# Kernel optimization log

Measured on AMD Instinct MI355X. Metric: run time of the kernel, lower is better.

The kernel has to match this reference:

```python
import jax, jax.numpy as jnp
import numpy as np

N_STEPS = 5


def setup_inputs() -> dict:
    key = jax.random.key(0)
    ks = jax.random.split(key, 12)
    B, N, E, D = 4, 2048, 2, 128
    prop_state = jax.random.normal(ks[0], (B, N, D), dtype=jnp.float32)
    A = (jax.random.uniform(ks[1], (B, N, 2 * N * E)) < 0.01).astype(jnp.float32)
    s = 0.02  # init scale from _initialization
    W_in = jax.random.normal(ks[2], (E, D, D), dtype=jnp.float32) * s
    b_in = jax.random.normal(ks[3], (E, D), dtype=jnp.float32) * s
    W_out = jax.random.normal(ks[4], (E, D, D), dtype=jnp.float32) * s
    b_out = jax.random.normal(ks[5], (E, D), dtype=jnp.float32) * s
    W_r = jax.random.normal(ks[6], (3 * D, D), dtype=jnp.float32) * s
    b_r = jax.random.normal(ks[7], (D,), dtype=jnp.float32) * s
    W_z = jax.random.normal(ks[8], (3 * D, D), dtype=jnp.float32) * s
    b_z = jax.random.normal(ks[9], (D,), dtype=jnp.float32) * s
    W_h = jax.random.normal(ks[10], (3 * D, D), dtype=jnp.float32) * s
    b_h = jax.random.normal(ks[11], (D,), dtype=jnp.float32) * s
    return {"prop_state": prop_state, "A": A, "W_in": W_in, "b_in": b_in,
            "W_out": W_out, "b_out": b_out, "W_r": W_r, "b_r": b_r,
            "W_z": W_z, "b_z": b_z, "W_h": W_h, "b_h": b_h}


def _ggnn_forward(prop_state, A, W_in, b_in, W_out, b_out,
                  W_r, b_r, W_z, b_z, W_h, b_h):
    B, N, D = prop_state.shape
    E = W_in.shape[0]
    A_in = A[:, :, : N * E]    # [B, N, N*E]
    A_out = A[:, :, N * E:]    # [B, N, N*E]
    h = prop_state
    for _ in range(N_STEPS):
        # per-edge-type projections, node-major / edge-type-minor ordering
        ins = (jnp.einsum('bnd,edf->bnef', h, W_in) + b_in).reshape(B, N * E, D)
        outs = (jnp.einsum('bnd,edf->bnef', h, W_out) + b_out).reshape(B, N * E, D)
        a_in = jnp.einsum('bnm,bmd->bnd', A_in, ins)    # [B, N, D]
        a_out = jnp.einsum('bnm,bmd->bnd', A_out, outs)  # [B, N, D]
        a = jnp.concatenate([a_in, a_out, h], axis=-1)   # [B, N, 3D]
        r = jax.nn.sigmoid(a @ W_r + b_r)
        z = jax.nn.sigmoid(a @ W_z + b_z)
        joined = jnp.concatenate([a_in, a_out, r * h], axis=-1)
        h_hat = jnp.tanh(joined @ W_h + b_h)
        h = (1.0 - z) * h + z * h_hat
    return h


def reference(prop_state, A, W_in, b_in, W_out, b_out,
              W_r, b_r, W_z, b_z, W_h, b_h):
    return _ggnn_forward(prop_state, A, W_in, b_in, W_out, b_out,
                         W_r, b_r, W_z, b_z, W_h, b_h)
```

## Files before the change

kernel.cpp:

```cpp
#include <hip/hip_runtime.h>
#include <stdint.h>

#define ROWS 8192
#define CAP 64
#define NSTEPS 5
#define ZROW 8192

typedef short bf16x8 __attribute__((ext_vector_type(8)));
typedef float f32x4 __attribute__((ext_vector_type(4)));
typedef unsigned short u16;
typedef unsigned int u32;

__device__ __forceinline__ float bf2f(u16 u){ union{u32 i; float f;} x; x.i=(u32)u<<16; return x.f; }
__device__ __forceinline__ u16 f2bf(float f){ union{float f; u32 i;} x; x.f=f; u32 r = x.i + 0x7fffu + ((x.i>>16)&1u); return (u16)(r>>16); }

#define MFMA __builtin_amdgcn_mfma_f32_16x16x32_bf16
#define SWZ(r, byte) ((byte) ^ (((r)&7)<<4))


__device__ __forceinline__ float wsel(const float* __restrict__ Wr, const float* __restrict__ Wz,
                                      const float* __restrict__ Wh, int f, int o){
  if (o < 128) return Wr[(size_t)f*128 + o];
  if (o < 256) return Wz[(size_t)f*128 + (o-128)];
  return (f < 256) ? Wh[(size_t)f*128 + (o-256)] : 0.f;
}

__global__ void k_prep(const float* __restrict__ prop, float* __restrict__ hf, u16* __restrict__ hbf,
                       const float* __restrict__ W_in, const float* __restrict__ b_in,
                       const float* __restrict__ W_out, const float* __restrict__ b_out,
                       const float* __restrict__ W_r, const float* __restrict__ W_z,
                       const float* __restrict__ W_h,
                       u16* __restrict__ WfT, float* __restrict__ bv, u16* __restrict__ WhbT)
{
  int bid = blockIdx.x;
  if (bid < 4096){
    int i = bid*256 + threadIdx.x;
    float v = prop[i]; hf[i] = v; hbf[i] = f2bf(v);
    return;
  }
  if (bid == 4096 && threadIdx.x < 128) hbf[(size_t)ZROW*128 + threadIdx.x] = 0;
  int i = (bid-4096)*256 + threadIdx.x;
  if (i < 640*384){
    int k = i/384, o = i - k*384;
    float s;
    if (k >= 512){
      s = wsel(W_r, W_z, W_h, 256 + (k-512), o);
    } else {
      const float* Wrow; int fb;
      if (k < 256){ Wrow = W_in  + (size_t)((k>>7)&1)*16384 + (size_t)(k&127)*128; fb = 0; }
      else { int kk = k-256; Wrow = W_out + (size_t)(kk>>7)*16384 + (size_t)(kk&127)*128; fb = 128; }
      s = 0.f;
#pragma unroll 8
      for (int f=0; f<128; f++) s += Wrow[f] * wsel(W_r, W_z, W_h, fb+f, o);
    }
    WfT[(size_t)o*640 + k] = f2bf(s);
  } else if (i < 640*384 + 4*384){
    int j = i - 640*384; int q = j / 384, o = j - q*384;
    const float* bp = (q < 2) ? (b_in + q*128) : (b_out + (q-2)*128);
    int fb = (q < 2) ? 0 : 128;
    float s = 0.f;
#pragma unroll 8
    for (int f=0; f<128; f++) s += bp[f] * wsel(W_r, W_z, W_h, fb+f, o);
    bv[j] = s;
  } else if (i < 640*384 + 4*384 + 128*128){
    int j = i - (640*384 + 4*384); int kk = j>>7, o = j&127;
    WhbT[(size_t)o*128 + kk] = f2bf(W_h[(size_t)(256+kk)*128 + o]);
  }
}

__global__ void k_csr(const float* __restrict__ A,
                      int* __restrict__ idx4, int* __restrict__ cnt4)
{
  __shared__ int scnt[4];
  __shared__ int slist[4][CAP];
  int row = blockIdx.x, tid = threadIdx.x;
  if (tid < 4) scnt[tid] = 0;
  __syncthreads();
  const float* ar = A + (size_t)row * 8192;
  int babs = (row>>11)<<11;
  for (int c = tid*4; c < 8192; c += 1024){
    float4 v = *reinterpret_cast<const float4*>(ar + c);
    float vv[4] = {v.x, v.y, v.z, v.w};
#pragma unroll
    for (int j=0;j<4;j++){
      if (vv[j] != 0.f){
        int m = c + j;
        int lst = ((m>>12)<<1) | (m&1);
        int n = (m & 4095) >> 1;
        int p = atomicAdd(&scnt[lst], 1);
        if (p < CAP) slist[lst][p] = babs | n;
      }
    }
  }
  __syncthreads();
  if (tid < 4) cnt4[(row<<2) + tid] = scnt[tid];
  for (int j = tid; j < 4*CAP; j += 256){
    int l = j>>6, p = j&63;
    int c = scnt[l]; if (c > CAP) c = CAP;
    if (p < c) idx4[(((size_t)(row<<2) + l)<<6) + p] = slist[l][p];
  }
}

__global__ __launch_bounds__(512) void k_fused(
    const int* __restrict__ cnt4, const int* __restrict__ idx4,
    const u16* __restrict__ WfT, const float* __restrict__ bv,
    const float* __restrict__ b_r, const float* __restrict__ b_z, const float* __restrict__ b_h,
    const u16* __restrict__ WhbT, float* __restrict__ hf, u16* __restrict__ hbf)
{
  __shared__ u16  X_s[32*512];
  __shared__ u16  rh_s[32*128];
  __shared__ u16  z_s[32*128];
  __shared__ u16  hh_s[32*128];
  __shared__ int  cnts[32][4];

  int tid  = threadIdx.x;
  int wave = tid>>6, lane = tid&63, lr = lane&15, lk = lane>>4;
  int m0 = blockIdx.x*32;

  if (tid < 128) cnts[tid>>2][tid&3] = cnt4[((m0 + (tid>>2))<<2) + (tid&3)];

  const u16* hb = hbf + (lane<<1);
#pragma unroll
  for (int p=0; p<2; p++){
    int base_l = p*64 + wave*8;
    int cc[8], my[8];
#pragma unroll
    for (int j=0;j<8;j++){
      int l = base_l + j;
      int lid = ((m0 + (l>>2))<<2) | (l&3);
      int c = cnt4[lid]; if (c > CAP) c = CAP;
      cc[j] = c;
      my[j] = (lane < c) ? idx4[((size_t)lid<<6) + lane] : ZROW;
    }
    int cmax = 0;
#pragma unroll
    for (int j=0;j<8;j++) cmax = max(cmax, cc[j]);

    float a0[8] = {0,0,0,0,0,0,0,0}, a1[8] = {0,0,0,0,0,0,0,0};
    u32 v[8];
#pragma unroll
    for (int j=0;j<8;j++){
      int n = __shfl(my[j], 0);
      v[j] = *reinterpret_cast<const u32*>(hb + ((size_t)n<<7));
    }
    for (int i=1; i<cmax; i++){
      u32 vn[8];
#pragma unroll
      for (int j=0;j<8;j++){
        int n = __shfl(my[j], i);
        vn[j] = *reinterpret_cast<const u32*>(hb + ((size_t)n<<7));
      }
#pragma unroll
      for (int j=0;j<8;j++){
        union{u32 u; float f;} lo, hi;
        lo.u = v[j]<<16; hi.u = v[j] & 0xffff0000u;
        a0[j] += lo.f; a1[j] += hi.f;
        v[j] = vn[j];
      }
    }
    if (cmax > 0){
#pragma unroll
      for (int j=0;j<8;j++){
        union{u32 u; float f;} lo, hi;
        lo.u = v[j]<<16; hi.u = v[j] & 0xffff0000u;
        a0[j] += lo.f; a1[j] += hi.f;
      }
    }
#pragma unroll
    for (int j=0;j<8;j++){
      int l = base_l + j, rl = l>>2, q = l&3;
      u32 pk = ((u32)f2bf(a1[j])<<16) | (u32)f2bf(a0[j]);
      *reinterpret_cast<u32*>((char*)X_s + SWZ(rl, rl*1024 + q*256 + lane*4)) = pk;
    }
  }
  __syncthreads();

  int n0 = wave*48;
  f32x4 acc[2][3] = {};
  const u16* Ah = hbf + (size_t)(m0+lr)*128 + lk*8;
  const u16* Bw = WfT + (size_t)(n0+lr)*640 + lk*8;
#pragma unroll
  for (int k=0;k<512;k+=32){
    bf16x8 b0 = *reinterpret_cast<const bf16x8*>(Bw + k);
    bf16x8 b1 = *reinterpret_cast<const bf16x8*>(Bw + 16*640 + k);
    bf16x8 b2 = *reinterpret_cast<const bf16x8*>(Bw + 32*640 + k);
#pragma unroll
    for (int mt=0;mt<2;mt++){
      int row = mt*16 + lr;
      bf16x8 a = *reinterpret_cast<const bf16x8*>((const char*)X_s + SWZ(row, row*1024 + (k + lk*8)*2));
      acc[mt][0] = MFMA(a, b0, acc[mt][0], 0,0,0);
      acc[mt][1] = MFMA(a, b1, acc[mt][1], 0,0,0);
      acc[mt][2] = MFMA(a, b2, acc[mt][2], 0,0,0);
    }
  }
#pragma unroll
  for (int k=0;k<128;k+=32){
    bf16x8 b0 = *reinterpret_cast<const bf16x8*>(Bw + 512 + k);
    bf16x8 b1 = *reinterpret_cast<const bf16x8*>(Bw + 16*640 + 512 + k);
    bf16x8 b2 = *reinterpret_cast<const bf16x8*>(Bw + 32*640 + 512 + k);
#pragma unroll
    for (int mt=0;mt<2;mt++){
      bf16x8 a = *reinterpret_cast<const bf16x8*>(Ah + (size_t)mt*16*128 + k);
      acc[mt][0] = MFMA(a, b0, acc[mt][0], 0,0,0);
      acc[mt][1] = MFMA(a, b1, acc[mt][1], 0,0,0);
      acc[mt][2] = MFMA(a, b2, acc[mt][2], 0,0,0);
    }
  }

#pragma unroll
  for (int nt=0;nt<3;nt++){
    int oo = n0 + nt*16 + lr;
    float base = (oo<128) ? b_r[oo] : (oo<256) ? b_z[oo-128] : b_h[oo-256];
    float q0 = bv[oo], q1 = bv[384+oo], q2 = bv[768+oo], q3 = bv[1152+oo];
#pragma unroll
    for (int mt=0;mt<2;mt++){
#pragma unroll
      for (int i2=0;i2<4;i2++){
        int rl = mt*16 + lk*4 + i2;
        float v = acc[mt][nt][i2] + base
                + cnts[rl][0]*q0 + cnts[rl][1]*q1 + cnts[rl][2]*q2 + cnts[rl][3]*q3;
        if (oo < 128){
          float s = 1.f/(1.f + expf(-v));
          float hv = hf[(size_t)(m0+rl)*128 + oo];
          *reinterpret_cast<u16*>((char*)rh_s + SWZ(rl, rl*256 + oo*2)) = f2bf(s*hv);
        } else if (oo < 256){
          float s = 1.f/(1.f + expf(-v));
          z_s[rl*128 + (oo-128)] = (u16)(s*65535.f + 0.5f);
        } else {
          hh_s[rl*128 + (oo-256)] = f2bf(v);
        }
      }
    }
  }
  __syncthreads();

  int c0 = wave*16;
  f32x4 acc2[2] = {};
  const u16* Bh = WhbT + (size_t)(c0+lr)*128 + lk*8;
#pragma unroll
  for (int k=0;k<128;k+=32){
    bf16x8 b = *reinterpret_cast<const bf16x8*>(Bh + k);
#pragma unroll
    for (int mt=0;mt<2;mt++){
      int rr = mt*16 + lr;
      bf16x8 a = *reinterpret_cast<const bf16x8*>((char*)rh_s + SWZ(rr, rr*256 + (k + lk*8)*2));
      acc2[mt] = MFMA(a, b, acc2[mt], 0,0,0);
    }
  }

#pragma unroll
  for (int mt=0;mt<2;mt++){
#pragma unroll
    for (int i2=0;i2<4;i2++){
      int rl = mt*16 + lk*4 + i2, col = c0 + lr;
      size_t ix = (size_t)(m0+rl)*128 + col;
      float hhat = tanhf(acc2[mt][i2] + bf2f(hh_s[rl*128 + col]));
      float zz = (float)z_s[rl*128 + col] * (1.f/65535.f);
      float ho = hf[ix];
      float hn = ho + zz*(hhat - ho);
      hf[ix] = hn;
      hbf[ix] = f2bf(hn);
    }
  }
}


extern "C" void kernel_launch(void* const* d_in, const int* in_sizes, int n_in,
                              void* d_out, int out_size, void* d_ws, size_t ws_size,
                              hipStream_t stream)
{
  const float* prop  = (const float*)d_in[0];
  const float* A     = (const float*)d_in[1];
  const float* W_in  = (const float*)d_in[2];
  const float* b_in  = (const float*)d_in[3];
  const float* W_out = (const float*)d_in[4];
  const float* b_out = (const float*)d_in[5];
  const float* W_r   = (const float*)d_in[6];
  const float* b_r   = (const float*)d_in[7];
  const float* W_z   = (const float*)d_in[8];
  const float* b_z   = (const float*)d_in[9];
  const float* W_h   = (const float*)d_in[10];
  const float* b_h   = (const float*)d_in[11];

  char* ws = (char*)d_ws;
  size_t off = 0;
  auto nxt = [&](size_t bytes)->char*{ char* p = ws + off; off += (bytes + 255) & ~(size_t)255; return p; };
  int*   cnt4  = (int*)  nxt((size_t)ROWS*4*4);
  int*   idx4  = (int*)  nxt((size_t)ROWS*4*CAP*4);
  u16*   hbf   = (u16*)  nxt((size_t)(ROWS+1)*128*2);
  float* hf    = (float*)nxt((size_t)ROWS*128*4);
  u16*   WfT   = (u16*)  nxt((size_t)384*640*2);
  float* bv    = (float*)nxt((size_t)4*384*4);
  u16*   WhbT  = (u16*)  nxt((size_t)128*128*2);

  int fold_blocks = (640*384 + 4*384 + 128*128 + 255)/256;
  k_prep<<<4096 + fold_blocks, 256, 0, stream>>>(prop, hf, hbf,
      W_in, b_in, W_out, b_out, W_r, W_z, W_h, WfT, bv, WhbT);
  k_csr<<<ROWS, 256, 0, stream>>>(A, idx4, cnt4);

  for (int t=0; t<NSTEPS; t++){
    k_fused<<<ROWS/32, 512, 0, stream>>>(cnt4, idx4, WfT, bv, b_r, b_z, b_h, WhbT, hf, hbf);
  }

  hipMemcpyAsync(d_out, hf, (size_t)ROWS*128*4, hipMemcpyDeviceToDevice, stream);
}
```

Measured before the change: 334.2 us.

## Fuse all GGNN steps into one persistent kernel with a grid barrier

Replaces the five per-step kernel launches with a single persistent kernel of 256 blocks that loops over the steps and uses an atomic-counter grid barrier between them. The hidden state is double-buffered so no block reads rows another block is overwriting, and per-row edge counts are read from shared memory instead of global. This removes launch overhead and the gaps between launches, but the spin barrier depends on all 256 blocks being resident at once and adds serialization at each step.

```diff
diff --git a/kernel.cpp b/kernel.cpp
--- a/kernel.cpp
+++ b/kernel.cpp
@@ -5,6 +5,7 @@
 #define CAP 64
 #define NSTEPS 5
 #define ZROW 8192
+#define NBLK 256
 
 typedef short bf16x8 __attribute__((ext_vector_type(8)));
 typedef float f32x4 __attribute__((ext_vector_type(4)));
@@ -25,20 +26,28 @@
   return (f < 256) ? Wh[(size_t)f*128 + (o-256)] : 0.f;
 }
 
-__global__ void k_prep(const float* __restrict__ prop, float* __restrict__ hf, u16* __restrict__ hbf,
+__global__ void k_prep(const float* __restrict__ prop, float* __restrict__ hf0, u16* __restrict__ hbf0,
+                       u16* __restrict__ hbf1,
                        const float* __restrict__ W_in, const float* __restrict__ b_in,
                        const float* __restrict__ W_out, const float* __restrict__ b_out,
                        const float* __restrict__ W_r, const float* __restrict__ W_z,
                        const float* __restrict__ W_h,
-                       u16* __restrict__ WfT, float* __restrict__ bv, u16* __restrict__ WhbT)
+                       u16* __restrict__ WfT, float* __restrict__ bv, u16* __restrict__ WhbT,
+                       int* __restrict__ bar)
 {
   int bid = blockIdx.x;
   if (bid < 4096){
     int i = bid*256 + threadIdx.x;
-    float v = prop[i]; hf[i] = v; hbf[i] = f2bf(v);
+    float v = prop[i]; hf0[i] = v; hbf0[i] = f2bf(v);
     return;
   }
-  if (bid == 4096 && threadIdx.x < 128) hbf[(size_t)ZROW*128 + threadIdx.x] = 0;
+  if (bid == 4096){
+    if (threadIdx.x < 128){
+      hbf0[(size_t)ZROW*128 + threadIdx.x] = 0;
+      hbf1[(size_t)ZROW*128 + threadIdx.x] = 0;
+    }
+    if (threadIdx.x == 255) bar[0] = 0;
+  }
   int i = (bid-4096)*256 + threadIdx.x;
   if (i < 640*384){
     int k = i/384, o = i - k*384;
@@ -101,11 +110,26 @@
   }
 }
 
-__global__ __launch_bounds__(512) void k_fused(
+__device__ __forceinline__ void grid_sync(int* bar, int target){
+  __syncthreads();
+  if (threadIdx.x == 0){
+    __threadfence();
+    __hip_atomic_fetch_add(bar, 1, __ATOMIC_RELEASE, __HIP_MEMORY_SCOPE_AGENT);
+    while (__hip_atomic_fetch_add(bar, 0, __ATOMIC_RELAXED, __HIP_MEMORY_SCOPE_AGENT) < target)
+      __builtin_amdgcn_s_sleep(4);
+    __threadfence();
+  }
+  __syncthreads();
+}
+
+__global__ __launch_bounds__(512) void k_steps(
     const int* __restrict__ cnt4, const int* __restrict__ idx4,
     const u16* __restrict__ WfT, const float* __restrict__ bv,
     const float* __restrict__ b_r, const float* __restrict__ b_z, const float* __restrict__ b_h,
-    const u16* __restrict__ WhbT, float* __restrict__ hf, u16* __restrict__ hbf)
+    const u16* __restrict__ WhbT,
+    float* __restrict__ hf0, float* __restrict__ hf1,
+    u16* __restrict__ hbf0, u16* __restrict__ hbf1,
+    int* __restrict__ bar)
 {
   __shared__ u16  X_s[32*512];
   __shared__ u16  rh_s[32*128];
@@ -118,149 +142,159 @@
   int m0 = blockIdx.x*32;
 
   if (tid < 128) cnts[tid>>2][tid&3] = cnt4[((m0 + (tid>>2))<<2) + (tid&3)];
-
-  const u16* hb = hbf + (lane<<1);
-#pragma unroll
-  for (int p=0; p<2; p++){
-    int base_l = p*64 + wave*8;
-    int cc[8], my[8];
-#pragma unroll
-    for (int j=0;j<8;j++){
-      int l = base_l + j;
-      int lid = ((m0 + (l>>2))<<2) | (l&3);
-      int c = cnt4[lid]; if (c > CAP) c = CAP;
-      cc[j] = c;
-      my[j] = (lane < c) ? idx4[((size_t)lid<<6) + lane] : ZROW;
-    }
-    int cmax = 0;
-#pragma unroll
-    for (int j=0;j<8;j++) cmax = max(cmax, cc[j]);
-
-    float a0[8] = {0,0,0,0,0,0,0,0}, a1[8] = {0,0,0,0,0,0,0,0};
-    u32 v[8];
-#pragma unroll
-    for (int j=0;j<8;j++){
-      int n = __shfl(my[j], 0);
-      v[j] = *reinterpret_cast<const u32*>(hb + ((size_t)n<<7));
-    }
-    for (int i=1; i<cmax; i++){
-      u32 vn[8];
+  __syncthreads();
+
+  for (int step=0; step<NSTEPS; step++){
+    const u16*  hbf_r = (step&1) ? hbf1 : hbf0;
+    u16*        hbf_w = (step&1) ? hbf0 : hbf1;
+    const float* hf_r = (step&1) ? hf1 : hf0;
+    float*       hf_w = (step&1) ? hf0 : hf1;
+
+    const u16* hb = hbf_r + (lane<<1);
+#pragma unroll
+    for (int p=0; p<2; p++){
+      int base_l = p*64 + wave*8;
+      int cc[8], my[8];
 #pragma unroll
       for (int j=0;j<8;j++){
-        int n = __shfl(my[j], i);
-        vn[j] = *reinterpret_cast<const u32*>(hb + ((size_t)n<<7));
-      }
+        int l = base_l + j;
+        int c = cnts[l>>2][l&3]; if (c > CAP) c = CAP;
+        cc[j] = c;
+        int lid = ((m0 + (l>>2))<<2) | (l&3);
+        my[j] = (lane < c) ? idx4[((size_t)lid<<6) + lane] : ZROW;
+      }
+      int cmax = 0;
+#pragma unroll
+      for (int j=0;j<8;j++) cmax = max(cmax, cc[j]);
+
+      float a0[8] = {0,0,0,0,0,0,0,0}, a1[8] = {0,0,0,0,0,0,0,0};
+      u32 v[8];
 #pragma unroll
       for (int j=0;j<8;j++){
-        union{u32 u; float f;} lo, hi;
-        lo.u = v[j]<<16; hi.u = v[j] & 0xffff0000u;
-        a0[j] += lo.f; a1[j] += hi.f;
-        v[j] = vn[j];
-      }
-    }
-    if (cmax > 0){
+        int n = __shfl(my[j], 0);
+        v[j] = *reinterpret_cast<const u32*>(hb + ((size_t)n<<7));
+      }
+      for (int i=1; i<cmax; i++){
+        u32 vn[8];
+#pragma unroll
+        for (int j=0;j<8;j++){
+          int n = __shfl(my[j], i);
+          vn[j] = *reinterpret_cast<const u32*>(hb + ((size_t)n<<7));
+        }
+#pragma unroll
+        for (int j=0;j<8;j++){
+          union{u32 u; float f;} lo, hi;
+          lo.u = v[j]<<16; hi.u = v[j] & 0xffff0000u;
+          a0[j] += lo.f; a1[j] += hi.f;
+          v[j] = vn[j];
+        }
+      }
+      if (cmax > 0){
+#pragma unroll
+        for (int j=0;j<8;j++){
+          union{u32 u; float f;} lo, hi;
+          lo.u = v[j]<<16; hi.u = v[j] & 0xffff0000u;
+          a0[j] += lo.f; a1[j] += hi.f;
+        }
+      }
 #pragma unroll
       for (int j=0;j<8;j++){
-        union{u32 u; float f;} lo, hi;
-        lo.u = v[j]<<16; hi.u = v[j] & 0xffff0000u;
-        a0[j] += lo.f; a1[j] += hi.f;
-      }
-    }
-#pragma unroll
-    for (int j=0;j<8;j++){
-      int l = base_l + j, rl = l>>2, q = l&3;
-      u32 pk = ((u32)f2bf(a1[j])<<16) | (u32)f2bf(a0[j]);
-      *reinterpret_cast<u32*>((char*)X_s + SWZ(rl, rl*1024 + q*256 + lane*4)) = pk;
-    }
-  }
-  __syncthreads();
-
-  int n0 = wave*48;
-  f32x4 acc[2][3] = {};
-  const u16* Ah = hbf + (size_t)(m0+lr)*128 + lk*8;
-  const u16* Bw = WfT + (size_t)(n0+lr)*640 + lk*8;
-#pragma unroll
-  for (int k=0;k<512;k+=32){
-    bf16x8 b0 = *reinterpret_cast<const bf16x8*>(Bw + k);
-    bf16x8 b1 = *reinterpret_cast<const bf16x8*>(Bw + 16*640 + k);
-    bf16x8 b2 = *reinterpret_cast<const bf16x8*>(Bw + 32*640 + k);
+        int l = base_l + j, rl = l>>2, q = l&3;
+        u32 pk = ((u32)f2bf(a1[j])<<16) | (u32)f2bf(a0[j]);
+        *reinterpret_cast<u32*>((char*)X_s + SWZ(rl, rl*1024 + q*256 + lane*4)) = pk;
+      }
+    }
+    __syncthreads();
+
+    int n0 = wave*48;
+    f32x4 acc[2][3] = {};
+    const u16* Ah = hbf_r + (size_t)(m0+lr)*128 + lk*8;
+    const u16* Bw = WfT + (size_t)(n0+lr)*640 + lk*8;
+#pragma unroll
+    for (int k=0;k<512;k+=32){
+      bf16x8 b0 = *reinterpret_cast<const bf16x8*>(Bw + k);
+      bf16x8 b1 = *reinterpret_cast<const bf16x8*>(Bw + 16*640 + k);
+      bf16x8 b2 = *reinterpret_cast<const bf16x8*>(Bw + 32*640 + k);
+#pragma unroll
+      for (int mt=0;mt<2;mt++){
+        int row = mt*16 + lr;
+        bf16x8 a = *reinterpret_cast<const bf16x8*>((const char*)X_s + SWZ(row, row*1024 + (k + lk*8)*2));
+        acc[mt][0] = MFMA(a, b0, acc[mt][0], 0,0,0);
+        acc[mt][1] = MFMA(a, b1, acc[mt][1], 0,0,0);
+        acc[mt][2] = MFMA(a, b2, acc[mt][2], 0,0,0);
+      }
+    }
+#pragma unroll
+    for (int k=0;k<128;k+=32){
+      bf16x8 b0 = *reinterpret_cast<const bf16x8*>(Bw + 512 + k);
+      bf16x8 b1 = *reinterpret_cast<const bf16x8*>(Bw + 16*640 + 512 + k);
+      bf16x8 b2 = *reinterpret_cast<const bf16x8*>(Bw + 32*640 + 512 + k);
+#pragma unroll
+      for (int mt=0;mt<2;mt++){
+        bf16x8 a = *reinterpret_cast<const bf16x8*>(Ah + (size_t)mt*16*128 + k);
+        acc[mt][0] = MFMA(a, b0, acc[mt][0], 0,0,0);
+        acc[mt][1] = MFMA(a, b1, acc[mt][1], 0,0,0);
+        acc[mt][2] = MFMA(a, b2, acc[mt][2], 0,0,0);
+      }
+    }
+
+#pragma unroll
+    for (int nt=0;nt<3;nt++){
+      int oo = n0 + nt*16 + lr;
+      float base = (oo<128) ? b_r[oo] : (oo<256) ? b_z[oo-128] : b_h[oo-256];
+      float q0 = bv[oo], q1 = bv[384+oo], q2 = bv[768+oo], q3 = bv[1152+oo];
+#pragma unroll
+      for (int mt=0;mt<2;mt++){
+#pragma unroll
+        for (int i2=0;i2<4;i2++){
+          int rl = mt*16 + lk*4 + i2;
+          float v = acc[mt][nt][i2] + base
+                  + cnts[rl][0]*q0 + cnts[rl][1]*q1 + cnts[rl][2]*q2 + cnts[rl][3]*q3;
+          if (oo < 128){
+            float s = 1.f/(1.f + expf(-v));
+            float hv = hf_r[(size_t)(m0+rl)*128 + oo];
+            *reinterpret_cast<u16*>((char*)rh_s + SWZ(rl, rl*256 + oo*2)) = f2bf(s*hv);
+          } else if (oo < 256){
+            float s = 1.f/(1.f + expf(-v));
+            z_s[rl*128 + (oo-128)] = (u16)(s*65535.f + 0.5f);
+          } else {
+            hh_s[rl*128 + (oo-256)] = f2bf(v);
+          }
+        }
+      }
+    }
+    __syncthreads();
+
+    int c0 = wave*16;
+    f32x4 acc2[2] = {};
+    const u16* Bh = WhbT + (size_t)(c0+lr)*128 + lk*8;
+#pragma unroll
+    for (int k=0;k<128;k+=32){
+      bf16x8 b = *reinterpret_cast<const bf16x8*>(Bh + k);
+#pragma unroll
+      for (int mt=0;mt<2;mt++){
+        int rr = mt*16 + lr;
+        bf16x8 a = *reinterpret_cast<const bf16x8*>((char*)rh_s + SWZ(rr, rr*256 + (k + lk*8)*2));
+        acc2[mt] = MFMA(a, b, acc2[mt], 0,0,0);
+      }
+    }
+
 #pragma unroll
     for (int mt=0;mt<2;mt++){
-      int row = mt*16 + lr;
-      bf16x8 a = *reinterpret_cast<const bf16x8*>((const char*)X_s + SWZ(row, row*1024 + (k + lk*8)*2));
-      acc[mt][0] = MFMA(a, b0, acc[mt][0], 0,0,0);
-      acc[mt][1] = MFMA(a, b1, acc[mt][1], 0,0,0);
-      acc[mt][2] = MFMA(a, b2, acc[mt][2], 0,0,0);
-    }
-  }
-#pragma unroll
-  for (int k=0;k<128;k+=32){
-    bf16x8 b0 = *reinterpret_cast<const bf16x8*>(Bw + 512 + k);
-    bf16x8 b1 = *reinterpret_cast<const bf16x8*>(Bw + 16*640 + 512 + k);
-    bf16x8 b2 = *reinterpret_cast<const bf16x8*>(Bw + 32*640 + 512 + k);
-#pragma unroll
-    for (int mt=0;mt<2;mt++){
-      bf16x8 a = *reinterpret_cast<const bf16x8*>(Ah + (size_t)mt*16*128 + k);
-      acc[mt][0] = MFMA(a, b0, acc[mt][0], 0,0,0);
-      acc[mt][1] = MFMA(a, b1, acc[mt][1], 0,0,0);
-      acc[mt][2] = MFMA(a, b2, acc[mt][2], 0,0,0);
-    }
-  }
-
-#pragma unroll
-  for (int nt=0;nt<3;nt++){
-    int oo = n0 + nt*16 + lr;
-    float base = (oo<128) ? b_r[oo] : (oo<256) ? b_z[oo-128] : b_h[oo-256];
-    float q0 = bv[oo], q1 = bv[384+oo], q2 = bv[768+oo], q3 = bv[1152+oo];
-#pragma unroll
-    for (int mt=0;mt<2;mt++){
 #pragma unroll
       for (int i2=0;i2<4;i2++){
-        int rl = mt*16 + lk*4 + i2;
-        float v = acc[mt][nt][i2] + base
-                + cnts[rl][0]*q0 + cnts[rl][1]*q1 + cnts[rl][2]*q2 + cnts[rl][3]*q3;
-        if (oo < 128){
-          float s = 1.f/(1.f + expf(-v));
-          float hv = hf[(size_t)(m0+rl)*128 + oo];
-          *reinterpret_cast<u16*>((char*)rh_s + SWZ(rl, rl*256 + oo*2)) = f2bf(s*hv);
-        } else if (oo < 256){
-          float s = 1.f/(1.f + expf(-v));
-          z_s[rl*128 + (oo-128)] = (u16)(s*65535.f + 0.5f);
-        } else {
-          hh_s[rl*128 + (oo-256)] = f2bf(v);
-        }
-      }
-    }
-  }
-  __syncthreads();
-
-  int c0 = wave*16;
-  f32x4 acc2[2] = {};
-  const u16* Bh = WhbT + (size_t)(c0+lr)*128 + lk*8;
-#pragma unroll
-  for (int k=0;k<128;k+=32){
-    bf16x8 b = *reinterpret_cast<const bf16x8*>(Bh + k);
-#pragma unroll
-    for (int mt=0;mt<2;mt++){
-      int rr = mt*16 + lr;
-      bf16x8 a = *reinterpret_cast<const bf16x8*>((char*)rh_s + SWZ(rr, rr*256 + (k + lk*8)*2));
-      acc2[mt] = MFMA(a, b, acc2[mt], 0,0,0);
-    }
-  }
-
-#pragma unroll
-  for (int mt=0;mt<2;mt++){
-#pragma unroll
-    for (int i2=0;i2<4;i2++){
-      int rl = mt*16 + lk*4 + i2, col = c0 + lr;
-      size_t ix = (size_t)(m0+rl)*128 + col;
-      float hhat = tanhf(acc2[mt][i2] + bf2f(hh_s[rl*128 + col]));
-      float zz = (float)z_s[rl*128 + col] * (1.f/65535.f);
-      float ho = hf[ix];
-      float hn = ho + zz*(hhat - ho);
-      hf[ix] = hn;
-      hbf[ix] = f2bf(hn);
-    }
+        int rl = mt*16 + lk*4 + i2, col = c0 + lr;
+        size_t ix = (size_t)(m0+rl)*128 + col;
+        float hhat = tanhf(acc2[mt][i2] + bf2f(hh_s[rl*128 + col]));
+        float zz = (float)z_s[rl*128 + col] * (1.f/65535.f);
+        float ho = hf_r[ix];
+        float hn = ho + zz*(hhat - ho);
+        hf_w[ix] = hn;
+        hbf_w[ix] = f2bf(hn);
+      }
+    }
+
+    if (step < NSTEPS-1) grid_sync(bar, NBLK*(step+1));
   }
 }
 
@@ -287,20 +321,22 @@
   auto nxt = [&](size_t bytes)->char*{ char* p = ws + off; off += (bytes + 255) & ~(size_t)255; return p; };
   int*   cnt4  = (int*)  nxt((size_t)ROWS*4*4);
   int*   idx4  = (int*)  nxt((size_t)ROWS*4*CAP*4);
-  u16*   hbf   = (u16*)  nxt((size_t)(ROWS+1)*128*2);
-  float* hf    = (float*)nxt((size_t)ROWS*128*4);
+  u16*   hbf0  = (u16*)  nxt((size_t)(ROWS+1)*128*2);
+  u16*   hbf1  = (u16*)  nxt((size_t)(ROWS+1)*128*2);
+  float* hf0   = (float*)nxt((size_t)ROWS*128*4);
+  float* hf1   = (float*)nxt((size_t)ROWS*128*4);
   u16*   WfT   = (u16*)  nxt((size_t)384*640*2);
   float* bv    = (float*)nxt((size_t)4*384*4);
   u16*   WhbT  = (u16*)  nxt((size_t)128*128*2);
+  int*   bar   = (int*)  nxt(256);
 
   int fold_blocks = (640*384 + 4*384 + 128*128 + 255)/256;
-  k_prep<<<4096 + fold_blocks, 256, 0, stream>>>(prop, hf, hbf,
-      W_in, b_in, W_out, b_out, W_r, W_z, W_h, WfT, bv, WhbT);
+  k_prep<<<4096 + fold_blocks, 256, 0, stream>>>(prop, hf0, hbf0, hbf1,
+      W_in, b_in, W_out, b_out, W_r, W_z, W_h, WfT, bv, WhbT, bar);
   k_csr<<<ROWS, 256, 0, stream>>>(A, idx4, cnt4);
 
-  for (int t=0; t<NSTEPS; t++){
-    k_fused<<<ROWS/32, 512, 0, stream>>>(cnt4, idx4, WfT, bv, b_r, b_z, b_h, WhbT, hf, hbf);
-  }
-
-  hipMemcpyAsync(d_out, hf, (size_t)ROWS*128*4, hipMemcpyDeviceToDevice, stream);
-}
+  k_steps<<<NBLK, 512, 0, stream>>>(cnt4, idx4, WfT, bv, b_r, b_z, b_h, WhbT,
+                                    hf0, hf1, hbf0, hbf1, bar);
+
+  hipMemcpyAsync(d_out, hf1, (size_t)ROWS*128*4, hipMemcpyDeviceToDevice, stream);
+}
```

New measurement: 649.0 us. 94.2% more time.
